# Kernel tuning notes

Hardware: AMD Instinct MI355X
Metric: run time of the kernel (lower is better)

The kernel has to match this reference:

```python
import jax, jax.numpy as jnp
import numpy as np

IN, HID = 1024, 1024
B, T = 64, 512

def _linear_params(key, fan_in, fan_out):
    # torch nn.Linear default init: U(-1/sqrt(fan_in), 1/sqrt(fan_in))
    k1, k2 = jax.random.split(key)
    bound = 1.0 / np.sqrt(fan_in)
    W = jax.random.uniform(k1, (fan_in, fan_out), minval=-bound, maxval=bound, dtype=jnp.float32)
    b = jax.random.uniform(k2, (fan_out,), minval=-bound, maxval=bound, dtype=jnp.float32)
    return W, b

def setup_inputs() -> dict:
    key = jax.random.key(0)
    keys = jax.random.split(key, 7)
    inputs = jax.random.normal(keys[0], (B, T, IN), dtype=jnp.float32)
    W_ir, b_ir = _linear_params(keys[1], IN, HID)
    W_hr, b_hr = _linear_params(keys[2], HID, HID)
    W_iz, b_iz = _linear_params(keys[3], IN, HID)
    W_hz, b_hz = _linear_params(keys[4], HID, HID)
    W_in, b_in = _linear_params(keys[5], IN, HID)
    W_hn, b_hn = _linear_params(keys[6], HID, HID)
    return dict(inputs=inputs,
                W_ir=W_ir, b_ir=b_ir, W_hr=W_hr, b_hr=b_hr,
                W_iz=W_iz, b_iz=b_iz, W_hz=W_hz, b_hz=b_hz,
                W_in=W_in, b_in=b_in, W_hn=W_hn, b_hn=b_hn)

def reference(inputs, W_ir, b_ir, W_hr, b_hr, W_iz, b_iz, W_hz, b_hz, W_in, b_in, W_hn, b_hn):
    # time-major: [T, B, IN]
    x = jnp.transpose(inputs, (1, 0, 2))
    # precompute input-side projections in one batched GEMM each (same math)
    xr = jnp.einsum('tbi,ih->tbh', x, W_ir) + b_ir
    xz = jnp.einsum('tbi,ih->tbh', x, W_iz) + b_iz
    xn = jnp.einsum('tbi,ih->tbh', x, W_in) + b_in
    h0 = jnp.zeros((1, HID), dtype=inputs.dtype)  # broadcasts over batch like torch

    def step(h, gates):
        gr, gz, gn = gates
        r = jax.nn.sigmoid(gr + h @ W_hr + b_hr)
        z = jax.nn.sigmoid(gz + h @ W_hz + b_hz)
        n = jnp.tanh(gn + r * (h @ W_hn + b_hn))
        h_new = (1.0 - z) * n + z * h
        return h_new, h_new

    h_t, output = jax.lax.scan(step, jnp.broadcast_to(h0, (x.shape[1], HID)), (xr, xz, xn))
    return output, h_t
```

## Files before the change

kernel.cpp:

```cpp
#include <hip/hip_runtime.h>
#include <cstdint>
#include <cstddef>

#define TT   512
#define BATCH 64
#define HID  1024
#define KDIM 1024

typedef short bf16x8 __attribute__((ext_vector_type(8)));
typedef float f32x4 __attribute__((ext_vector_type(4)));

__device__ __forceinline__ unsigned short f2b(float f) {
    unsigned int u = __float_as_uint(f);
    u = (u + 0x7fffu + ((u >> 16) & 1u)) >> 16;
    return (unsigned short)u;
}

__global__ __launch_bounds__(256) void k_init(
    const float* __restrict__ b_ir, const float* __restrict__ b_iz, const float* __restrict__ b_in,
    const float* __restrict__ b_hr, const float* __restrict__ b_hz, const float* __restrict__ b_hn,
    float* __restrict__ bias_x, float* __restrict__ bias_h,
    unsigned short* __restrict__ hbf, int* __restrict__ flags)
{
    int gid = blockIdx.x * 256 + threadIdx.x;
    if (gid < HID) {
        bias_x[gid]        = b_ir[gid];
        bias_x[HID + gid]  = b_iz[gid];
        bias_x[2*HID + gid]= b_in[gid];
        bias_h[gid]        = b_hr[gid];
        bias_h[HID + gid]  = b_hz[gid];
        bias_h[2*HID + gid]= b_hn[gid];
    }
    ushort4 z4 = make_ushort4(0, 0, 0, 0);
    ushort4* p = reinterpret_cast<ushort4*>(hbf);
    p[2*gid]   = z4;
    p[2*gid+1] = z4;
    if (gid < 256 * 16) flags[gid] = 0;
}

__global__ __launch_bounds__(256) void k_trans(
    const float* __restrict__ w0, const float* __restrict__ w1, const float* __restrict__ w2,
    const float* __restrict__ w3, const float* __restrict__ w4, const float* __restrict__ w5,
    unsigned short* __restrict__ wxT, unsigned short* __restrict__ whT)
{
    __shared__ float tile[32][33];
    int z = blockIdx.z;
    const float* src = (z == 0) ? w0 : (z == 1) ? w1 : (z == 2) ? w2
                     : (z == 3) ? w3 : (z == 4) ? w4 : w5;
    unsigned short* dst = (z < 3) ? (wxT + (size_t)z * HID * KDIM)
                                  : (whT + (size_t)(z - 3) * HID * KDIM);
    int kb = blockIdx.x * 32, jb = blockIdx.y * 32;
    int tx = threadIdx.x, ty = threadIdx.y;
    #pragma unroll
    for (int p = 0; p < 4; p++)
        tile[tx][ty + 8*p] = src[(size_t)(kb + ty + 8*p) * HID + jb + tx];
    __syncthreads();
    #pragma unroll
    for (int p = 0; p < 4; p++) {
        int n = jb + ty + 8*p;
        dst[(size_t)n * KDIM + kb + tx] = f2b(tile[ty + 8*p][tx]);
    }
}

#define BM 128
#define BN 128
#define LDA 72

__global__ __launch_bounds__(256, 2) void k_gemm_x(
    const float* __restrict__ x,
    const unsigned short* __restrict__ wxT,
    const float* __restrict__ biasx,
    float* __restrict__ ggr, float* __restrict__ ggz, float* __restrict__ ggn)
{
    __shared__ unsigned short lA[BM * LDA];
    __shared__ unsigned short lB[BN * LDA];
    int tid  = threadIdx.x;
    int wave = tid >> 6, lane = tid & 63;
    int l16  = lane & 15, lhi = lane >> 4;
    int rbase = blockIdx.x * BM;
    int nbase = blockIdx.y * BN;
    int wm = (wave >> 1) * 64, wn = (wave & 1) * 64;

    f32x4 acc[4][4];
    for (int a = 0; a < 4; a++)
        for (int b = 0; b < 4; b++)
            acc[a][b] = f32x4{0.f, 0.f, 0.f, 0.f};

    int arow = tid >> 4;
    int acol = (tid & 15) * 4;
    int brow = tid >> 3;
    int bcol = (tid & 7) * 8;

    for (int kb = 0; kb < KDIM; kb += 64) {
        __syncthreads();
        #pragma unroll
        for (int p = 0; p < 8; p++) {
            int r = p * 16 + arow;
            float4 v = *(const float4*)(x + (size_t)(rbase + r) * KDIM + kb + acol);
            ushort4 s;
            s.x = f2b(v.x); s.y = f2b(v.y); s.z = f2b(v.z); s.w = f2b(v.w);
            *(ushort4*)(lA + r * LDA + acol) = s;
        }
        #pragma unroll
        for (int p = 0; p < 4; p++) {
            int r = p * 32 + brow;
            bf16x8 v = *(const bf16x8*)(wxT + (size_t)(nbase + r) * KDIM + kb + bcol);
            *(bf16x8*)(lB + r * LDA + bcol) = v;
        }
        __syncthreads();
        #pragma unroll
        for (int kk = 0; kk < 2; kk++) {
            bf16x8 af[4], bfr[4];
            #pragma unroll
            for (int mt = 0; mt < 4; mt++)
                af[mt] = *(const bf16x8*)(lA + (wm + mt*16 + l16) * LDA + kk*32 + lhi*8);
            #pragma unroll
            for (int nt = 0; nt < 4; nt++)
                bfr[nt] = *(const bf16x8*)(lB + (wn + nt*16 + l16) * LDA + kk*32 + lhi*8);
            #pragma unroll
            for (int mt = 0; mt < 4; mt++)
                #pragma unroll
                for (int nt = 0; nt < 4; nt++)
                    acc[mt][nt] = __builtin_amdgcn_mfma_f32_16x16x32_bf16(
                        af[mt], bfr[nt], acc[mt][nt], 0, 0, 0);
        }
    }
    #pragma unroll
    for (int nt = 0; nt < 4; nt++) {
        int n = nbase + wn + nt*16 + l16;
        float bv = biasx[n];
        int g = n >> 10;
        int j = n & 1023;
        float* outp = (g == 0) ? ggr : (g == 1) ? ggz : ggn;
        #pragma unroll
        for (int mt = 0; mt < 4; mt++) {
            #pragma unroll
            for (int i = 0; i < 4; i++) {
                int R = rbase + wm + mt*16 + lhi*4 + i;
                size_t orow = (size_t)((R & 511) * BATCH + (R >> 9));
                outp[orow * HID + j] = acc[mt][nt][i] + bv;
            }
        }
    }
}

__global__ __launch_bounds__(256, 1) void k_recur(
    const float* __restrict__ ggr, const float* __restrict__ ggz,
    float* __restrict__ dout,
    const unsigned short* __restrict__ whT,
    const float* __restrict__ biash,
    unsigned short* __restrict__ hbf,
    int* __restrict__ flags)
{
    __shared__ float red[3 * 4 * 64 * 4];
    __shared__ unsigned long long hsu[64];
    unsigned short* hsp = (unsigned short*)hsu;

    int tid  = threadIdx.x;
    int w    = tid >> 6, lane = tid & 63;
    int l16  = lane & 15, lhi = lane >> 4;
    int blk  = blockIdx.x;
    int q    = blk & 3;
    int c    = blk >> 2;
    int row  = tid >> 4;
    int col  = tid & 15;
    int j_l  = c * 16 + l16;
    int j_t  = c * 16 + col;
    int b_t  = q * 16 + row;
    int kbase = w * 256 + lhi * 8;

    int* myflag = &flags[((w * 16 + l16) * 4 + q) * 16];

    bf16x8 wr[8], wz[8], wn[8];
    {
        const unsigned short* base = whT + (size_t)j_l * KDIM + kbase;
        #pragma unroll
        for (int kk = 0; kk < 8; kk++) {
            wr[kk] = *(const bf16x8*)(base + kk*32);
            wz[kk] = *(const bf16x8*)(base + kk*32 + (size_t)HID * KDIM);
            wn[kk] = *(const bf16x8*)(base + kk*32 + (size_t)2 * HID * KDIM);
        }
    }
    float bhr = biash[j_t], bhz = biash[HID + j_t], bhn = biash[2*HID + j_t];

    float hp = 0.f;
    float cgr, cgz, cgn;
    {
        size_t g0 = (size_t)b_t * HID + j_t;
        cgr = ggr[g0]; cgz = ggz[g0]; cgn = dout[g0];
    }

    #pragma unroll 1
    for (int t = 0; t < TT; t++) {
        if (t > 0) {
            bool ok;
            do {
                int f = __hip_atomic_load(myflag, __ATOMIC_RELAXED, __HIP_MEMORY_SCOPE_AGENT);
                ok = (f >= t);
            } while (!__all(ok));
        }

        const unsigned short* hb = hbf + (size_t)(t & 1) * BATCH * HID
                                 + (size_t)(q * 16 + l16) * HID + kbase;
        unsigned long long hu[16];
        #pragma unroll
        for (int kk = 0; kk < 8; kk++) {
            hu[2*kk]   = __hip_atomic_load((unsigned long long*)(hb + kk*32),
                                           __ATOMIC_RELAXED, __HIP_MEMORY_SCOPE_AGENT);
            hu[2*kk+1] = __hip_atomic_load((unsigned long long*)(hb + kk*32) + 1,
                                           __ATOMIC_RELAXED, __HIP_MEMORY_SCOPE_AGENT);
        }

        float ngr = 0.f, ngz = 0.f, ngn = 0.f;
        if (t + 1 < TT) {
            size_t g1 = (size_t)((t + 1) * BATCH + b_t) * HID + j_t;
            ngr = ggr[g1]; ngz = ggz[g1]; ngn = dout[g1];
        }

        f32x4 a0{0.f,0.f,0.f,0.f}, a1{0.f,0.f,0.f,0.f}, a2{0.f,0.f,0.f,0.f};
        #pragma unroll
        for (int kk = 0; kk < 8; kk++) {
            union { unsigned long long u[2]; bf16x8 v; } fa;
            fa.u[0] = hu[2*kk]; fa.u[1] = hu[2*kk+1];
            a0 = __builtin_amdgcn_mfma_f32_16x16x32_bf16(fa.v, wr[kk], a0, 0, 0, 0);
            a1 = __builtin_amdgcn_mfma_f32_16x16x32_bf16(fa.v, wz[kk], a1, 0, 0, 0);
            a2 = __builtin_amdgcn_mfma_f32_16x16x32_bf16(fa.v, wn[kk], a2, 0, 0, 0);
        }

        {
            f32x4* rp = (f32x4*)red;
            rp[(0*4 + w) * 64 + lane] = a0;
            rp[(1*4 + w) * 64 + lane] = a1;
            rp[(2*4 + w) * 64 + lane] = a2;
        }
        __syncthreads();
        int lsrc = (row >> 2) * 16 + col, ri = row & 3;
        float s0 = 0.f, s1 = 0.f, s2 = 0.f;
        #pragma unroll
        for (int ww = 0; ww < 4; ww++) {
            s0 += red[((0*4 + ww) * 64 + lsrc) * 4 + ri];
            s1 += red[((1*4 + ww) * 64 + lsrc) * 4 + ri];
            s2 += red[((2*4 + ww) * 64 + lsrc) * 4 + ri];
        }

        float r  = 1.f / (1.f + __expf(-(cgr + s0 + bhr)));
        float z  = 1.f / (1.f + __expf(-(cgz + s1 + bhz)));
        float nv = cgn + r * (s2 + bhn);
        float th = 1.f - 2.f / (1.f + __expf(2.f * nv));
        float hv = (1.f - z) * th + z * hp;
        hp = hv;
        dout[((size_t)t * BATCH + b_t) * HID + j_t] = hv;
        if (t == TT - 1) {
            dout[(size_t)TT * BATCH * HID + (size_t)b_t * HID + j_t] = hv;
            break;
        }
        cgr = ngr; cgz = ngz; cgn = ngn;

        hsp[row * 16 + col] = f2b(hv);
        __syncthreads();
        if (tid < 64) {
            int rr = tid >> 2, ch = tid & 3;
            unsigned long long v = hsu[rr * 4 + ch];
            unsigned long long* dst = (unsigned long long*)(
                hbf + (size_t)((t + 1) & 1) * BATCH * HID
                    + (size_t)(q * 16 + rr) * HID + c * 16 + ch * 4);
            __hip_atomic_store(dst, v, __ATOMIC_RELAXED, __HIP_MEMORY_SCOPE_AGENT);
            asm volatile("s_waitcnt vmcnt(0)" ::: "memory");
            if (tid == 0)
                __hip_atomic_store(&flags[blk * 16], t + 1,
                                   __ATOMIC_RELAXED, __HIP_MEMORY_SCOPE_AGENT);
        }
    }
}

extern "C" void kernel_launch(void* const* d_in, const int* in_sizes, int n_in,
                              void* d_out, int out_size, void* d_ws, size_t ws_size,
                              hipStream_t stream)
{
    const float* x    = (const float*)d_in[0];
    const float* W_ir = (const float*)d_in[1];
    const float* b_ir = (const float*)d_in[2];
    const float* W_hr = (const float*)d_in[3];
    const float* b_hr = (const float*)d_in[4];
    const float* W_iz = (const float*)d_in[5];
    const float* b_iz = (const float*)d_in[6];
    const float* W_hz = (const float*)d_in[7];
    const float* b_hz = (const float*)d_in[8];
    const float* W_in = (const float*)d_in[9];
    const float* b_in = (const float*)d_in[10];
    const float* W_hn = (const float*)d_in[11];
    const float* b_hn = (const float*)d_in[12];
    float* out = (float*)d_out;

    char* ws = (char*)d_ws;
    size_t off = 0;
    auto alloc = [&](size_t bytes) -> char* {
        char* p = ws + off;
        off += (bytes + 255) & ~(size_t)255;
        return p;
    };
    float*          ggr      = (float*)alloc((size_t)TT * BATCH * HID * 4);
    float*          ggz      = (float*)alloc((size_t)TT * BATCH * HID * 4);
    unsigned short* wxT      = (unsigned short*)alloc((size_t)3 * HID * KDIM * 2);
    unsigned short* whT      = (unsigned short*)alloc((size_t)3 * HID * KDIM * 2);
    float*          bias_x   = (float*)alloc(3 * HID * 4);
    float*          bias_h   = (float*)alloc(3 * HID * 4);
    unsigned short* hbf      = (unsigned short*)alloc((size_t)2 * BATCH * HID * 2);
    int*            flags    = (int*)alloc(256 * 16 * 4);

    k_init<<<64, 256, 0, stream>>>(b_ir, b_iz, b_in, b_hr, b_hz, b_hn,
                                   bias_x, bias_h, hbf, flags);
    k_trans<<<dim3(32, 32, 6), dim3(32, 8), 0, stream>>>(W_ir, W_iz, W_in,
                                                         W_hr, W_hz, W_hn, wxT, whT);
    k_gemm_x<<<dim3(256, 24), 256, 0, stream>>>(x, wxT, bias_x, ggr, ggz, out);
    k_recur<<<256, 256, 0, stream>>>(ggr, ggz, out, whT, bias_h, hbf, flags);
}
```

Before: 2.825 ms.

## Repartition recurrent blocks into batch groups with dynamic rank and narrower flag polling

```diff
diff --git a/kernel.cpp b/kernel.cpp
--- a/kernel.cpp
+++ b/kernel.cpp
@@ -20,7 +20,7 @@
     const float* __restrict__ b_ir, const float* __restrict__ b_iz, const float* __restrict__ b_in,
     const float* __restrict__ b_hr, const float* __restrict__ b_hz, const float* __restrict__ b_hn,
     float* __restrict__ bias_x, float* __restrict__ bias_h,
-    unsigned short* __restrict__ hbf, int* __restrict__ flags)
+    unsigned short* __restrict__ hbf, int* __restrict__ flags, int* __restrict__ gcnt)
 {
     int gid = blockIdx.x * 256 + threadIdx.x;
     if (gid < HID) {
@@ -36,6 +36,7 @@
     p[2*gid]   = z4;
     p[2*gid+1] = z4;
     if (gid < 256 * 16) flags[gid] = 0;
+    if (gid < 16) gcnt[gid] = 0;
 }
 
 __global__ __launch_bounds__(256) void k_trans(
@@ -150,37 +151,50 @@
     const unsigned short* __restrict__ whT,
     const float* __restrict__ biash,
     unsigned short* __restrict__ hbf,
-    int* __restrict__ flags)
-{
-    __shared__ float red[3 * 4 * 64 * 4];
+    int* __restrict__ flags,
+    int* __restrict__ gcnt)
+{
+    __shared__ f32x4 red[6 * 4 * 64];
     __shared__ unsigned long long hsu[64];
+    __shared__ int shr[1];
     unsigned short* hsp = (unsigned short*)hsu;
 
     int tid  = threadIdx.x;
+    if (tid == 0) shr[0] = atomicAdd(gcnt, 1);
+    __syncthreads();
+    int grank = shr[0];
+    int grp   = (grank >> 5) & 7;
+    int rank  = grank & 31;
+
     int w    = tid >> 6, lane = tid & 63;
     int l16  = lane & 15, lhi = lane >> 4;
-    int blk  = blockIdx.x;
-    int q    = blk & 3;
-    int c    = blk >> 2;
-    int row  = tid >> 4;
-    int col  = tid & 15;
-    int j_l  = c * 16 + l16;
-    int j_t  = c * 16 + col;
-    int b_t  = q * 16 + row;
+    int row  = tid >> 5;
+    int col  = tid & 31;
+    int colbase = rank * 32;
+    int b_t  = grp * 8 + row;
+    int j_t  = colbase + col;
+    int hrow = grp * 8 + (l16 & 7);
     int kbase = w * 256 + lhi * 8;
 
-    int* myflag = &flags[((w * 16 + l16) * 4 + q) * 16];
-
-    bf16x8 wr[8], wz[8], wn[8];
-    {
-        const unsigned short* base = whT + (size_t)j_l * KDIM + kbase;
-        #pragma unroll
-        for (int kk = 0; kk < 8; kk++) {
-            wr[kk] = *(const bf16x8*)(base + kk*32);
-            wz[kk] = *(const bf16x8*)(base + kk*32 + (size_t)HID * KDIM);
-            wn[kk] = *(const bf16x8*)(base + kk*32 + (size_t)2 * HID * KDIM);
-        }
-    }
+    bf16x8 wf[2][3][8];
+    #pragma unroll
+    for (int ct = 0; ct < 2; ct++)
+        #pragma unroll
+        for (int g = 0; g < 3; g++) {
+            const unsigned short* base =
+                whT + (size_t)(g * HID + colbase + ct * 16 + l16) * KDIM + kbase;
+            #pragma unroll
+            for (int kk = 0; kk < 8; kk++)
+                wf[ct][g][kk] = *(const bf16x8*)(base + kk * 32);
+        }
+    #pragma unroll
+    for (int ct = 0; ct < 2; ct++)
+        #pragma unroll
+        for (int g = 0; g < 3; g++)
+            #pragma unroll
+            for (int kk = 0; kk < 8; kk++)
+                asm volatile("" : "+v"(wf[ct][g][kk]));
+
     float bhr = biash[j_t], bhz = biash[HID + j_t], bhn = biash[2*HID + j_t];
 
     float hp = 0.f;
@@ -190,18 +204,22 @@
         cgr = ggr[g0]; cgz = ggz[g0]; cgn = dout[g0];
     }
 
+    int* pollp  = flags + (size_t)(grp * 32 + w * 8 + (lane & 7)) * 16;
+    int* myflag = flags + (size_t)(grp * 32 + rank) * 16;
+
     #pragma unroll 1
     for (int t = 0; t < TT; t++) {
         if (t > 0) {
+            int guard = 0;
             bool ok;
             do {
-                int f = __hip_atomic_load(myflag, __ATOMIC_RELAXED, __HIP_MEMORY_SCOPE_AGENT);
+                int f = __hip_atomic_load(pollp, __ATOMIC_RELAXED, __HIP_MEMORY_SCOPE_AGENT);
                 ok = (f >= t);
-            } while (!__all(ok));
+            } while (!__all(ok) && ++guard < (1 << 17));
         }
 
         const unsigned short* hb = hbf + (size_t)(t & 1) * BATCH * HID
-                                 + (size_t)(q * 16 + l16) * HID + kbase;
+                                 + (size_t)hrow * HID + kbase;
         unsigned long long hu[16];
         #pragma unroll
         for (int kk = 0; kk < 8; kk++) {
@@ -217,30 +235,38 @@
             ngr = ggr[g1]; ngz = ggz[g1]; ngn = dout[g1];
         }
 
-        f32x4 a0{0.f,0.f,0.f,0.f}, a1{0.f,0.f,0.f,0.f}, a2{0.f,0.f,0.f,0.f};
+        f32x4 acc[2][3];
+        #pragma unroll
+        for (int ct = 0; ct < 2; ct++)
+            #pragma unroll
+            for (int g = 0; g < 3; g++)
+                acc[ct][g] = f32x4{0.f, 0.f, 0.f, 0.f};
         #pragma unroll
         for (int kk = 0; kk < 8; kk++) {
             union { unsigned long long u[2]; bf16x8 v; } fa;
             fa.u[0] = hu[2*kk]; fa.u[1] = hu[2*kk+1];
-            a0 = __builtin_amdgcn_mfma_f32_16x16x32_bf16(fa.v, wr[kk], a0, 0, 0, 0);
-            a1 = __builtin_amdgcn_mfma_f32_16x16x32_bf16(fa.v, wz[kk], a1, 0, 0, 0);
-            a2 = __builtin_amdgcn_mfma_f32_16x16x32_bf16(fa.v, wn[kk], a2, 0, 0, 0);
-        }
-
-        {
-            f32x4* rp = (f32x4*)red;
-            rp[(0*4 + w) * 64 + lane] = a0;
-            rp[(1*4 + w) * 64 + lane] = a1;
-            rp[(2*4 + w) * 64 + lane] = a2;
-        }
+            #pragma unroll
+            for (int ct = 0; ct < 2; ct++)
+                #pragma unroll
+                for (int g = 0; g < 3; g++)
+                    acc[ct][g] = __builtin_amdgcn_mfma_f32_16x16x32_bf16(
+                        fa.v, wf[ct][g][kk], acc[ct][g], 0, 0, 0);
+        }
+
+        #pragma unroll
+        for (int ct = 0; ct < 2; ct++)
+            #pragma unroll
+            for (int g = 0; g < 3; g++)
+                red[((g * 2 + ct) * 4 + w) * 64 + lane] = acc[ct][g];
         __syncthreads();
-        int lsrc = (row >> 2) * 16 + col, ri = row & 3;
+        int ctt = col >> 4, ri = row & 3;
+        int lsrc = (row >> 2) * 16 + (col & 15);
         float s0 = 0.f, s1 = 0.f, s2 = 0.f;
         #pragma unroll
         for (int ww = 0; ww < 4; ww++) {
-            s0 += red[((0*4 + ww) * 64 + lsrc) * 4 + ri];
-            s1 += red[((1*4 + ww) * 64 + lsrc) * 4 + ri];
-            s2 += red[((2*4 + ww) * 64 + lsrc) * 4 + ri];
+            s0 += red[((0 * 2 + ctt) * 4 + ww) * 64 + lsrc][ri];
+            s1 += red[((1 * 2 + ctt) * 4 + ww) * 64 + lsrc][ri];
+            s2 += red[((2 * 2 + ctt) * 4 + ww) * 64 + lsrc][ri];
         }
 
         float r  = 1.f / (1.f + __expf(-(cgr + s0 + bhr)));
@@ -256,18 +282,18 @@
         }
         cgr = ngr; cgz = ngz; cgn = ngn;
 
-        hsp[row * 16 + col] = f2b(hv);
+        hsp[row * 32 + col] = f2b(hv);
         __syncthreads();
         if (tid < 64) {
-            int rr = tid >> 2, ch = tid & 3;
-            unsigned long long v = hsu[rr * 4 + ch];
+            int rr = tid >> 3, ch = tid & 7;
+            unsigned long long v = hsu[rr * 8 + ch];
             unsigned long long* dst = (unsigned long long*)(
                 hbf + (size_t)((t + 1) & 1) * BATCH * HID
-                    + (size_t)(q * 16 + rr) * HID + c * 16 + ch * 4);
+                    + (size_t)(grp * 8 + rr) * HID + colbase + ch * 4);
             __hip_atomic_store(dst, v, __ATOMIC_RELAXED, __HIP_MEMORY_SCOPE_AGENT);
             asm volatile("s_waitcnt vmcnt(0)" ::: "memory");
             if (tid == 0)
-                __hip_atomic_store(&flags[blk * 16], t + 1,
+                __hip_atomic_store(myflag, t + 1,
                                    __ATOMIC_RELAXED, __HIP_MEMORY_SCOPE_AGENT);
         }
     }
@@ -307,11 +333,12 @@
     float*          bias_h   = (float*)alloc(3 * HID * 4);
     unsigned short* hbf      = (unsigned short*)alloc((size_t)2 * BATCH * HID * 2);
     int*            flags    = (int*)alloc(256 * 16 * 4);
+    int*            gcnt     = (int*)alloc(16 * 4);
 
     k_init<<<64, 256, 0, stream>>>(b_ir, b_iz, b_in, b_hr, b_hz, b_hn,
-                                   bias_x, bias_h, hbf, flags);
+                                   bias_x, bias_h, hbf, flags, gcnt);
     k_trans<<<dim3(32, 32, 6), dim3(32, 8), 0, stream>>>(W_ir, W_iz, W_in,
                                                          W_hr, W_hz, W_hn, wxT, whT);
     k_gemm_x<<<dim3(256, 24), 256, 0, stream>>>(x, wxT, bias_x, ggr, ggz, out);
-    k_recur<<<256, 256, 0, stream>>>(ggr, ggz, out, whT, bias_h, hbf, flags);
-}
+    k_recur<<<256, 256, 0, stream>>>(ggr, ggz, out, whT, bias_h, hbf, flags, gcnt);
+}
```

After: 2.839 ms. No clear change (+0.5%).
